# Optimization experiments

Measured on AMD Instinct MI355X. Metric: run time of the kernel, lower is better.

The kernel has to match this reference:

```python
import jax, jax.numpy as jnp
import numpy as np

E = 1_000_000   # number of metapath instances (edges)
H = 8           # num_heads
D = 32          # out_feats per head
N = 100_000     # number of dst nodes
NEG_SLOPE = 0.01


def setup_inputs() -> dict:
    key = jax.random.key(0)
    k1, k2, k3 = jax.random.split(key, 3)
    h_meta = jax.random.normal(k1, (E, H * D), dtype=jnp.float32)
    attn_r = jax.random.normal(k2, (1, H, D), dtype=jnp.float32)
    dst = jnp.sort(jax.random.randint(k3, (E,), 0, N, dtype=jnp.int32))
    return {"h_meta": h_meta, "attn_r": attn_r, "dst": dst, "num_nodes": N}


def reference(h_meta, attn_r, dst, num_nodes):
    # h: [E, H, D]  (feat_drop is identity in eval mode)
    h = h_meta.reshape(-1, H, D)
    # er = (h * attn_r).sum(-1): per-edge, per-head attention logit  [E, H]
    er = jnp.sum(h * attn_r, axis=-1)
    e = jax.nn.leaky_relu(er, NEG_SLOPE)
    # edge_softmax grouped by destination node (numerically stable)
    m = jax.ops.segment_max(e, dst, num_segments=num_nodes, indices_are_sorted=True)  # [N, H]
    a = jnp.exp(e - m[dst])                                                           # [E, H]
    s = jax.ops.segment_sum(a, dst, num_segments=num_nodes, indices_are_sorted=True)  # [N, H]
    a = a / s[dst]
    # u_mul_e + sum reduce: weighted aggregation of edge features into dst nodes
    out = jax.ops.segment_sum(h * a[:, :, None], dst, num_segments=num_nodes,
                              indices_are_sorted=True)                               # [N, H, D]
    out = jax.nn.elu(out)
    return out.reshape(num_nodes, H * D)
```

## Files before the change

### kernel.cpp

```cpp
#include <hip/hip_runtime.h>
#include <math.h>


constexpr int H = 8;
constexpr int D = 32;
constexpr int HD = H * D;
constexpr float NEG_SLOPE = 0.01f;

__global__ __launch_bounds__(256) void magnn_fused(
    const float* __restrict__ h_meta,
    const float* __restrict__ attn_r,
    const int*   __restrict__ dst,
    float*       __restrict__ out,
    int E, int N)
{
    const int node = blockIdx.x * (blockDim.x >> 6) + (threadIdx.x >> 6);
    const int lane = threadIdx.x & 63;
    if (node >= N) return;

    int lo = 0, hi = E;
    while (lo < hi) {
        int mid = (lo + hi) >> 1;
        if (dst[mid] < node) lo = mid + 1; else hi = mid;
    }
    const int start = lo;
    hi = E;
    while (lo < hi) {
        int mid = (lo + hi) >> 1;
        if (dst[mid] <= node) lo = mid + 1; else hi = mid;
    }
    const int end = lo;

    const float4 ar = reinterpret_cast<const float4*>(attn_r)[lane];

    float  m = -INFINITY;
    float  l = 0.0f;
    float4 acc = make_float4(0.0f, 0.0f, 0.0f, 0.0f);

    const float4* __restrict__ hrow = reinterpret_cast<const float4*>(h_meta);

    for (int e = start; e < end; ++e) {
        const float4 hv = hrow[e * 64 + lane];
        float part = hv.x * ar.x + hv.y * ar.y + hv.z * ar.z + hv.w * ar.w;
        part += __shfl_xor(part, 1);
        part += __shfl_xor(part, 2);
        part += __shfl_xor(part, 4);
        const float el = part > 0.0f ? part : NEG_SLOPE * part;
        const float mn = fmaxf(m, el);
        const float sc = __expf(m - mn);
        const float p  = __expf(el - mn);
        l = l * sc + p;
        acc.x = acc.x * sc + p * hv.x;
        acc.y = acc.y * sc + p * hv.y;
        acc.z = acc.z * sc + p * hv.z;
        acc.w = acc.w * sc + p * hv.w;
        m = mn;
    }

    const float inv = (l > 0.0f) ? 1.0f / l : 0.0f;
    float4 o;
    o.x = acc.x * inv;
    o.y = acc.y * inv;
    o.z = acc.z * inv;
    o.w = acc.w * inv;
    o.x = o.x > 0.0f ? o.x : expm1f(o.x);
    o.y = o.y > 0.0f ? o.y : expm1f(o.y);
    o.z = o.z > 0.0f ? o.z : expm1f(o.z);
    o.w = o.w > 0.0f ? o.w : expm1f(o.w);

    reinterpret_cast<float4*>(out)[node * 64 + lane] = o;
}

extern "C" void kernel_launch(void* const* d_in, const int* in_sizes, int n_in,
                              void* d_out, int out_size, void* d_ws, size_t ws_size,
                              hipStream_t stream) {
    const float* h_meta = (const float*)d_in[0];
    const float* attn_r = (const float*)d_in[1];
    const int*   dst    = (const int*)d_in[2];
    float*       out    = (float*)d_out;

    const int E = in_sizes[2];
    const int N = out_size / HD;

    const int waves_per_block = 4;
    const int grid = (N + waves_per_block - 1) / waves_per_block;
    magnn_fused<<<grid, 256, 0, stream>>>(h_meta, attn_r, dst, out, E, N);
}
```

Before: 1.427 ms.

## Precompute CSR node offsets and split online softmax into two independent chains

```diff
diff --git a/kernel.cpp b/kernel.cpp
--- a/kernel.cpp
+++ b/kernel.cpp
@@ -2,45 +2,44 @@
 #include <math.h>
 
 
-constexpr int H = 8;
-constexpr int D = 32;
-constexpr int HD = H * D;
+constexpr int HD = 256;
 constexpr float NEG_SLOPE = 0.01f;
+
+__global__ __launch_bounds__(256) void build_starts(
+    const int* __restrict__ dst, int* __restrict__ starts, int E, int N)
+{
+    const int i = blockIdx.x * blockDim.x + threadIdx.x;
+    if (i >= E) return;
+    const int d = dst[i];
+    const int p = (i == 0) ? -1 : dst[i - 1];
+    for (int n = p + 1; n <= d; ++n) starts[n] = i;
+    if (i == E - 1)
+        for (int n = d + 1; n <= N; ++n) starts[n] = E;
+}
 
 __global__ __launch_bounds__(256) void magnn_fused(
     const float* __restrict__ h_meta,
     const float* __restrict__ attn_r,
-    const int*   __restrict__ dst,
+    const int*   __restrict__ starts,
     float*       __restrict__ out,
-    int E, int N)
+    int N)
 {
-    const int node = blockIdx.x * (blockDim.x >> 6) + (threadIdx.x >> 6);
+    const int node = blockIdx.x * 4 + (threadIdx.x >> 6);
     const int lane = threadIdx.x & 63;
     if (node >= N) return;
 
-    int lo = 0, hi = E;
-    while (lo < hi) {
-        int mid = (lo + hi) >> 1;
-        if (dst[mid] < node) lo = mid + 1; else hi = mid;
-    }
-    const int start = lo;
-    hi = E;
-    while (lo < hi) {
-        int mid = (lo + hi) >> 1;
-        if (dst[mid] <= node) lo = mid + 1; else hi = mid;
-    }
-    const int end = lo;
+    const int s = starts[node];
+    const int e = starts[node + 1];
 
     const float4 ar = reinterpret_cast<const float4*>(attn_r)[lane];
-
-    float  m = -INFINITY;
-    float  l = 0.0f;
-    float4 acc = make_float4(0.0f, 0.0f, 0.0f, 0.0f);
-
     const float4* __restrict__ hrow = reinterpret_cast<const float4*>(h_meta);
 
-    for (int e = start; e < end; ++e) {
-        const float4 hv = hrow[e * 64 + lane];
+    float  m0 = -INFINITY, l0 = 0.0f;
+    float  m1 = -INFINITY, l1 = 0.0f;
+    float4 a0 = make_float4(0.f, 0.f, 0.f, 0.f);
+    float4 a1 = make_float4(0.f, 0.f, 0.f, 0.f);
+
+    auto update = [&](float& m, float& l, float4& a, const float4& hv) {
         float part = hv.x * ar.x + hv.y * ar.y + hv.z * ar.z + hv.w * ar.w;
         part += __shfl_xor(part, 1);
         part += __shfl_xor(part, 2);
@@ -50,19 +49,39 @@
         const float sc = __expf(m - mn);
         const float p  = __expf(el - mn);
         l = l * sc + p;
-        acc.x = acc.x * sc + p * hv.x;
-        acc.y = acc.y * sc + p * hv.y;
-        acc.z = acc.z * sc + p * hv.z;
-        acc.w = acc.w * sc + p * hv.w;
+        a.x = a.x * sc + p * hv.x;
+        a.y = a.y * sc + p * hv.y;
+        a.z = a.z * sc + p * hv.z;
+        a.w = a.w * sc + p * hv.w;
         m = mn;
+    };
+
+    int i = s;
+    for (; i + 2 <= e; i += 2) {
+        const float4 h0 = hrow[i * 64 + lane];
+        const float4 h1 = hrow[(i + 1) * 64 + lane];
+        update(m0, l0, a0, h0);
+        update(m1, l1, a1, h1);
+    }
+    if (i < e) {
+        const float4 h0 = hrow[i * 64 + lane];
+        update(m0, l0, a0, h0);
     }
 
+    const float mn = fmaxf(m0, m1);
+    const float s0 = (m0 > -INFINITY) ? __expf(m0 - mn) : 0.0f;
+    const float s1 = (m1 > -INFINITY) ? __expf(m1 - mn) : 0.0f;
+    const float l  = l0 * s0 + l1 * s1;
+
+    float4 o;
+    o.x = a0.x * s0 + a1.x * s1;
+    o.y = a0.y * s0 + a1.y * s1;
+    o.z = a0.z * s0 + a1.z * s1;
+    o.w = a0.w * s0 + a1.w * s1;
+
     const float inv = (l > 0.0f) ? 1.0f / l : 0.0f;
-    float4 o;
-    o.x = acc.x * inv;
-    o.y = acc.y * inv;
-    o.z = acc.z * inv;
-    o.w = acc.w * inv;
+    o.x *= inv; o.y *= inv; o.z *= inv; o.w *= inv;
+
     o.x = o.x > 0.0f ? o.x : expm1f(o.x);
     o.y = o.y > 0.0f ? o.y : expm1f(o.y);
     o.z = o.z > 0.0f ? o.z : expm1f(o.z);
@@ -82,7 +101,10 @@
     const int E = in_sizes[2];
     const int N = out_size / HD;
 
-    const int waves_per_block = 4;
-    const int grid = (N + waves_per_block - 1) / waves_per_block;
-    magnn_fused<<<grid, 256, 0, stream>>>(h_meta, attn_r, dst, out, E, N);
+    int* starts = (int*)d_ws;
+
+    build_starts<<<(E + 255) / 256, 256, 0, stream>>>(dst, starts, E, N);
+
+    const int grid = (N + 3) / 4;
+    magnn_fused<<<grid, 256, 0, stream>>>(h_meta, attn_r, starts, out, N);
 }
```

Measured after the change: 1.308 ms. -8.3%, faster.
